# Kernel optimization log

Hardware: AMD Instinct MI355X
Metric: run time of the kernel (lower is better)

Reference implementation:

```python
import jax, jax.numpy as jnp
import numpy as np

EPS = 1e-12  # F.normalize default eps


def _l2norm(x):
    n = jnp.linalg.norm(x, axis=-1, keepdims=True)
    return x / jnp.maximum(n, EPS)


def setup_inputs() -> dict:
    key = jax.random.key(0)
    ks = jax.random.split(key, 6)
    B, N, d = 1024, 131072, 256
    query = jax.random.normal(ks[0], (B, d), dtype=jnp.float32)
    keys = jax.random.normal(ks[1], (N, d), dtype=jnp.float32)
    values = jax.random.normal(ks[2], (N, d), dtype=jnp.float32)
    quality_scores = jax.random.uniform(ks[3], (N,), dtype=jnp.float32)
    W = jax.random.normal(ks[4], (d, d), dtype=jnp.float32) / np.sqrt(d)
    b = jnp.zeros((d,), dtype=jnp.float32)
    temperature = jnp.asarray(0.02, dtype=jnp.float32)
    return {"query": query, "keys": keys, "values": values,
            "quality_scores": quality_scores, "W": W, "b": b,
            "temperature": temperature, "top_k": 32}


def reference(query, keys, values, quality_scores, W, b, temperature, top_k):
    # query_transform: nn.Linear -> x @ W.T + b
    q_t = query @ W.T + b                      # [B, d]
    qn = _l2norm(q_t)                          # [B, d]
    kn = _l2norm(keys)                         # [N, d]
    sim = (qn @ kn.T) / temperature            # [B, N]
    sim = sim + quality_scores[None, :] * 0.1  # quality boost
    top_vals, indices = jax.lax.top_k(sim, top_k)   # [B, k]
    scores = jax.nn.softmax(top_vals, axis=-1)      # [B, k]
    retrieved_keys = keys[indices]             # [B, k, d] gather
    retrieved_values = values[indices]         # [B, k, d]
    weighted_keys = jnp.einsum('bk,bkd->bd', scores, retrieved_keys)[:, None, :]
    weighted_values = jnp.einsum('bk,bkd->bd', scores, retrieved_values)[:, None, :]
    return weighted_keys, weighted_values, scores
```

## Files before the change

### kernel.cpp

```cpp
#include <hip/hip_runtime.h>
#include <cstdint>
#include <cstddef>

#define B_Q   1024
#define N_K   131072
#define DIM   256
#define TOPK  32
#define EPSN  1e-12f

#define NRANGES 16
#define QGROUPS 16
#define QT      64
#define WQ      8
#define NT      1024
#define NTILES  8
#define CAP     160
#define FLUSH_AT 96

typedef unsigned long long u64;
typedef unsigned int u32;

__global__ __launch_bounds__(256) void qn_kernel(
    const float* __restrict__ query, const float* __restrict__ W,
    const float* __restrict__ b, float* __restrict__ qn) {
  const int row = blockIdx.x;
  const int j   = threadIdx.x;
  __shared__ float4 qrow[64];
  __shared__ float red[256];
  if (j < 64) qrow[j] = ((const float4*)(query + (size_t)row * DIM))[j];
  __syncthreads();
  const float4* W4 = (const float4*)(W + (size_t)j * DIM);
  float acc = b[j];
  #pragma unroll 8
  for (int kk = 0; kk < 64; ++kk) {
    float4 w = W4[kk];
    float4 qv = qrow[kk];
    acc = fmaf(qv.x, w.x, acc);
    acc = fmaf(qv.y, w.y, acc);
    acc = fmaf(qv.z, w.z, acc);
    acc = fmaf(qv.w, w.w, acc);
  }
  red[j] = acc * acc;
  __syncthreads();
  #pragma unroll
  for (int s = 128; s > 0; s >>= 1) {
    if (j < s) red[j] += red[j + s];
    __syncthreads();
  }
  float norm = sqrtf(red[0]);
  qn[(size_t)row * DIM + j] = acc / fmaxf(norm, EPSN);
}

__global__ __launch_bounds__(256) void knorm_kernel(
    const float* __restrict__ keys, const float* __restrict__ quality,
    const float* __restrict__ temperature,
    float* __restrict__ scale, float* __restrict__ boost) {
  const int tid = threadIdx.x;
  const int lane = tid & 63;
  const int row = blockIdx.x * 4 + (tid >> 6);
  float4 v = ((const float4*)(keys + (size_t)row * DIM))[lane];
  float ss = v.x * v.x + v.y * v.y + v.z * v.z + v.w * v.w;
  #pragma unroll
  for (int off = 32; off > 0; off >>= 1) ss += __shfl_xor(ss, off, 64);
  if (lane == 0) {
    float norm = sqrtf(ss);
    scale[row] = 1.0f / (fmaxf(norm, EPSN) * temperature[0]);
    boost[row] = 0.1f * quality[row];
  }
}

__device__ __attribute__((noinline)) float wave_extract(
    float2* list, int n, int lane, float2* gout) {
  float v0 = -INFINITY, v1 = -INFINITY, v2 = -INFINITY;
  float i0 = 0.f, i1 = 0.f, i2 = 0.f;
  if (lane < n)        { float2 e = list[lane];       v0 = e.x; i0 = e.y; }
  if (lane + 64 < n)   { float2 e = list[lane + 64];  v1 = e.x; i1 = e.y; }
  if (lane + 128 < n)  { float2 e = list[lane + 128]; v2 = e.x; i2 = e.y; }
  float m = -INFINITY;
  #pragma unroll 1
  for (int it = 0; it < TOPK; ++it) {
    float lm = fmaxf(v0, fmaxf(v1, v2));
    m = lm;
    #pragma unroll
    for (int off = 32; off > 0; off >>= 1) m = fmaxf(m, __shfl_xor(m, off, 64));
    u64 msk = __ballot(lm == m);
    int first = __ffsll((unsigned long long)msk) - 1;
    if (lane == first) {
      float2 e;
      if (v0 == lm)      { e = make_float2(v0, i0); v0 = -INFINITY; }
      else if (v1 == lm) { e = make_float2(v1, i1); v1 = -INFINITY; }
      else               { e = make_float2(v2, i2); v2 = -INFINITY; }
      if (gout) gout[it] = e; else list[it] = e;
    }
  }
  return m;
}

__device__ __forceinline__ void gload_lds16(const float* __restrict__ g, void* l) {
  __builtin_amdgcn_global_load_lds(
      (const __attribute__((address_space(1))) void*)g,
      (__attribute__((address_space(3))) void*)l, 16, 0, 0);
}

__device__ __forceinline__ void stage_chunk(
    const float* __restrict__ keys, long nbase, int tile, int chunk,
    float4* kb, int tid) {
  const long nrow0 = nbase + (long)tile * NT + tid;
  const float* s0 = keys + (nrow0 << 8) + (chunk << 2);
  gload_lds16(s0, kb + tid);
  gload_lds16(s0 + (512L << 8), kb + tid + 512);
}

__global__ __launch_bounds__(512, 2) void sim_topk_kernel(
    const float* __restrict__ qn, const float* __restrict__ keys,
    const float* __restrict__ scale, const float* __restrict__ boost,
    float2* __restrict__ glists,
    float2* __restrict__ partials)
{
  const int tid  = threadIdx.x;
  const int lane = tid & 63;
  const int wid  = __builtin_amdgcn_readfirstlane(tid >> 6);
  const int rg = blockIdx.x;
  const int qg = blockIdx.y;
  const int qbase = qg * QT + wid * WQ;
  const long nbase = (long)rg * (N_K / NRANGES);

  __shared__ float4 kbuf[2][NT];
  __shared__ float  qbuf[QT * DIM];
  __shared__ int cnt[QT];

  if (tid < QT) cnt[tid] = 0;

  {
    const float* qsrc = qn + (size_t)(qg * QT) * DIM;
    #pragma unroll
    for (int it = 0; it < 8; ++it)
      gload_lds16(qsrc + (size_t)(it * 512 + tid) * 4, qbuf + (it * 512 + tid) * 4);
  }
  int buf = 0;
  stage_chunk(keys, nbase, 0, 0, &kbuf[0][0], tid);

  float tau_r[WQ];
  #pragma unroll
  for (int qi = 0; qi < WQ; ++qi) tau_r[qi] = -INFINITY;
  float2* const mybase = glists + ((size_t)qbase * NRANGES + rg) * CAP;

  #pragma unroll 1
  for (int t = 0; t < NTILES; ++t) {
    float acc[WQ][16];
    #pragma unroll
    for (int qi = 0; qi < WQ; ++qi)
      #pragma unroll
      for (int j = 0; j < 16; ++j) acc[qi][j] = 0.f;

    #pragma unroll 1
    for (int c = 0; c < 64; ++c) {
      __syncthreads();
      if (c < 63)                stage_chunk(keys, nbase, t,     c + 1, &kbuf[buf ^ 1][0], tid);
      else if (t < NTILES - 1)   stage_chunk(keys, nbase, t + 1, 0,     &kbuf[buf ^ 1][0], tid);
      float4 qv[WQ];
      #pragma unroll
      for (int qi = 0; qi < WQ; ++qi)
        qv[qi] = *(const float4*)&qbuf[(wid * WQ + qi) * DIM + c * 4];
      #pragma unroll
      for (int j = 0; j < 16; ++j) {
        float4 kv = kbuf[buf][j * 64 + lane];
        #pragma unroll
        for (int qi = 0; qi < WQ; ++qi) {
          acc[qi][j] = fmaf(qv[qi].x, kv.x, acc[qi][j]);
          acc[qi][j] = fmaf(qv[qi].y, kv.y, acc[qi][j]);
          acc[qi][j] = fmaf(qv[qi].z, kv.z, acc[qi][j]);
          acc[qi][j] = fmaf(qv[qi].w, kv.w, acc[qi][j]);
        }
      }
      buf ^= 1;
    }

    const int ntile0 = t * NT;
    #pragma unroll
    for (int j = 0; j < 16; ++j) {
      const int nloc = ntile0 + j * 64 + lane;
      const long ng = nbase + nloc;
      const float sc = scale[ng];
      const float bo = boost[ng];
      bool any = false;
      #pragma unroll
      for (int qi = 0; qi < WQ; ++qi) {
        float v = fmaf(acc[qi][j], sc, bo);
        bool p = v > tau_r[qi];
        any |= p;
        if (p) {
          int pos = atomicAdd(&cnt[wid * WQ + qi], 1);
          mybase[(size_t)qi * NRANGES * CAP + pos] = make_float2(v, __int_as_float((int)ng));
        }
      }
      if (__any(any)) {
        #pragma unroll
        for (int qi = 0; qi < WQ; ++qi) {
          int cc = cnt[wid * WQ + qi];
          if (cc > FLUSH_AT) {
            tau_r[qi] = wave_extract(mybase + (size_t)qi * NRANGES * CAP, cc, lane, nullptr);
            if (lane == 0) cnt[wid * WQ + qi] = TOPK;
          }
        }
      }
    }
  }

  #pragma unroll 1
  for (int qi = 0; qi < WQ; ++qi) {
    float2* out = partials + ((size_t)(qbase + qi) * NRANGES + rg) * TOPK;
    wave_extract(mybase + (size_t)qi * NRANGES * CAP, cnt[wid * WQ + qi], lane, out);
  }
}

__device__ __forceinline__ u32 f2ord(float f) {
  u32 u = __float_as_uint(f);
  return (u & 0x80000000u) ? ~u : (u | 0x80000000u);
}
__device__ __forceinline__ float ord2f(u32 o) {
  u32 u = (o & 0x80000000u) ? (o ^ 0x80000000u) : ~o;
  return __uint_as_float(u);
}

__global__ __launch_bounds__(256) void merge_kernel(
    const float2* __restrict__ partials, const float* __restrict__ keys,
    const float* __restrict__ values, float* __restrict__ out) {
  const int q = blockIdx.x;
  const int tid = threadIdx.x;
  __shared__ u64 skey[NRANGES * TOPK];
  for (int i = tid; i < 512; i += 256) {
    float2 e = partials[(size_t)q * 512 + i];
    int idx = __float_as_int(e.y);
    skey[i] = ((u64)f2ord(e.x) << 32) | (u32)(~(u32)idx);
  }
  __syncthreads();
  for (int k = 2; k <= 512; k <<= 1) {
    for (int jj = k >> 1; jj > 0; jj >>= 1) {
      for (int i = tid; i < 512; i += 256) {
        int ixj = i ^ jj;
        if (ixj > i) {
          u64 a = skey[i], bb = skey[ixj];
          bool up = ((i & k) == 0);
          if ((a < bb) == up) { skey[i] = bb; skey[ixj] = a; }
        }
      }
      __syncthreads();
    }
  }
  __shared__ float sval[TOPK];
  __shared__ int   sidx[TOPK];
  __shared__ float sscore[TOPK];
  if (tid < TOPK) {
    u64 kk = skey[tid];
    sval[tid] = ord2f((u32)(kk >> 32));
    sidx[tid] = (int)(~(u32)(kk & 0xffffffffu));
  }
  __syncthreads();
  if (tid < TOPK) {
    float m = sval[0];
    float e = expf(sval[tid] - m);
    float s = e;
    #pragma unroll
    for (int off = 16; off > 0; off >>= 1) s += __shfl_xor(s, off, 64);
    sscore[tid] = e / s;
  }
  __syncthreads();
  if (tid < TOPK) out[(size_t)2 * B_Q * DIM + (size_t)q * TOPK + tid] = sscore[tid];
  float wk = 0.f, wv = 0.f;
  #pragma unroll 4
  for (int kk2 = 0; kk2 < TOPK; ++kk2) {
    float s = sscore[kk2];
    size_t idr = (size_t)sidx[kk2] * DIM + tid;
    wk = fmaf(s, keys[idr], wk);
    wv = fmaf(s, values[idr], wv);
  }
  out[(size_t)q * DIM + tid] = wk;
  out[(size_t)B_Q * DIM + (size_t)q * DIM + tid] = wv;
}

extern "C" void kernel_launch(void* const* d_in, const int* in_sizes, int n_in,
                              void* d_out, int out_size, void* d_ws, size_t ws_size,
                              hipStream_t stream) {
  const float* query   = (const float*)d_in[0];
  const float* keys    = (const float*)d_in[1];
  const float* values  = (const float*)d_in[2];
  const float* quality = (const float*)d_in[3];
  const float* W       = (const float*)d_in[4];
  const float* b       = (const float*)d_in[5];
  const float* temp    = (const float*)d_in[6];
  float* out = (float*)d_out;
  float* ws = (float*)d_ws;

  float* qn    = ws;
  float* scale = ws + 262144;
  float* boost = ws + 393216;
  float2* partials = (float2*)(ws + 524288);
  float2* glists   = (float2*)(ws + 524288 + 1048576);

  hipLaunchKernelGGL(qn_kernel, dim3(B_Q), dim3(256), 0, stream, query, W, b, qn);
  hipLaunchKernelGGL(knorm_kernel, dim3(N_K / 4), dim3(256), 0, stream,
                     keys, quality, temp, scale, boost);
  hipLaunchKernelGGL(sim_topk_kernel, dim3(NRANGES, QGROUPS), dim3(512), 0, stream,
                     qn, keys, scale, boost, glists, partials);
  hipLaunchKernelGGL(merge_kernel, dim3(B_Q), dim3(256), 0, stream,
                     partials, keys, values, out);
}
```

Baseline: 2.060 ms.

## Shrink sim-topk tiles to 32 queries x 512 keys with 256-thread blocks

Reshapes the similarity/top-k kernel so each block handles 32 queries and 512-key tiles with 256 threads. Each pipeline phase now stages two 4-float chunks (8 dims), which halves the number of barriers per tile, and the accumulator array per thread shrinks from 16 to 8 keys per query. The grid doubles in the query dimension, giving more blocks and lower register pressure, but each key tile is now reloaded by twice as many query groups, doubling key traffic from global memory.

Result: faster. 1.994 ms (-3.2%).

```diff
diff --git a/kernel.cpp b/kernel.cpp
--- a/kernel.cpp
+++ b/kernel.cpp
@@ -9,11 +9,11 @@
 #define EPSN  1e-12f
 
 #define NRANGES 16
-#define QGROUPS 16
-#define QT      64
+#define QGROUPS 32
+#define QT      32
 #define WQ      8
-#define NT      1024
-#define NTILES  8
+#define NT      512
+#define NTILES  16
 #define CAP     160
 #define FLUSH_AT 96
 
@@ -102,16 +102,19 @@
       (__attribute__((address_space(3))) void*)l, 16, 0, 0);
 }
 
-__device__ __forceinline__ void stage_chunk(
-    const float* __restrict__ keys, long nbase, int tile, int chunk,
+__device__ __forceinline__ void stage_phase(
+    const float* __restrict__ keys, long nbase, int t, int c,
     float4* kb, int tid) {
-  const long nrow0 = nbase + (long)tile * NT + tid;
-  const float* s0 = keys + (nrow0 << 8) + (chunk << 2);
-  gload_lds16(s0, kb + tid);
-  gload_lds16(s0 + (512L << 8), kb + tid + 512);
-}
-
-__global__ __launch_bounds__(512, 2) void sim_topk_kernel(
+  #pragma unroll
+  for (int i = 0; i < 4; ++i) {
+    const int c2   = i >> 1;
+    const int keyl = (i & 1) * 256 + tid;
+    const float* src = keys + ((size_t)(nbase + t * NT + keyl) << 8) + c * 8 + c2 * 4;
+    gload_lds16(src, kb + c2 * 512 + keyl);
+  }
+}
+
+__global__ __launch_bounds__(256, 2) void sim_topk_kernel(
     const float* __restrict__ qn, const float* __restrict__ keys,
     const float* __restrict__ scale, const float* __restrict__ boost,
     float2* __restrict__ glists,
@@ -123,9 +126,10 @@
   const int rg = blockIdx.x;
   const int qg = blockIdx.y;
   const int qbase = qg * QT + wid * WQ;
+  const int qloc0 = wid * WQ;
   const long nbase = (long)rg * (N_K / NRANGES);
 
-  __shared__ float4 kbuf[2][NT];
+  __shared__ float4 kbuf4[2][2 * NT];
   __shared__ float  qbuf[QT * DIM];
   __shared__ int cnt[QT];
 
@@ -135,10 +139,10 @@
     const float* qsrc = qn + (size_t)(qg * QT) * DIM;
     #pragma unroll
     for (int it = 0; it < 8; ++it)
-      gload_lds16(qsrc + (size_t)(it * 512 + tid) * 4, qbuf + (it * 512 + tid) * 4);
+      gload_lds16(qsrc + (size_t)(it * 256 + tid) * 4, qbuf + (it * 256 + tid) * 4);
   }
   int buf = 0;
-  stage_chunk(keys, nbase, 0, 0, &kbuf[0][0], tid);
+  stage_phase(keys, nbase, 0, 0, &kbuf4[0][0], tid);
 
   float tau_r[WQ];
   #pragma unroll
@@ -147,30 +151,33 @@
 
   #pragma unroll 1
   for (int t = 0; t < NTILES; ++t) {
-    float acc[WQ][16];
+    float acc[WQ][8];
     #pragma unroll
     for (int qi = 0; qi < WQ; ++qi)
       #pragma unroll
-      for (int j = 0; j < 16; ++j) acc[qi][j] = 0.f;
+      for (int j = 0; j < 8; ++j) acc[qi][j] = 0.f;
 
     #pragma unroll 1
-    for (int c = 0; c < 64; ++c) {
+    for (int c = 0; c < 32; ++c) {
       __syncthreads();
-      if (c < 63)                stage_chunk(keys, nbase, t,     c + 1, &kbuf[buf ^ 1][0], tid);
-      else if (t < NTILES - 1)   stage_chunk(keys, nbase, t + 1, 0,     &kbuf[buf ^ 1][0], tid);
-      float4 qv[WQ];
+      if (c < 31)                stage_phase(keys, nbase, t,     c + 1, &kbuf4[buf ^ 1][0], tid);
+      else if (t < NTILES - 1)   stage_phase(keys, nbase, t + 1, 0,     &kbuf4[buf ^ 1][0], tid);
       #pragma unroll
-      for (int qi = 0; qi < WQ; ++qi)
-        qv[qi] = *(const float4*)&qbuf[(wid * WQ + qi) * DIM + c * 4];
-      #pragma unroll
-      for (int j = 0; j < 16; ++j) {
-        float4 kv = kbuf[buf][j * 64 + lane];
+      for (int c2 = 0; c2 < 2; ++c2) {
+        float4 qv[WQ];
         #pragma unroll
-        for (int qi = 0; qi < WQ; ++qi) {
-          acc[qi][j] = fmaf(qv[qi].x, kv.x, acc[qi][j]);
-          acc[qi][j] = fmaf(qv[qi].y, kv.y, acc[qi][j]);
-          acc[qi][j] = fmaf(qv[qi].z, kv.z, acc[qi][j]);
-          acc[qi][j] = fmaf(qv[qi].w, kv.w, acc[qi][j]);
+        for (int qi = 0; qi < WQ; ++qi)
+          qv[qi] = *(const float4*)&qbuf[(qloc0 + qi) * DIM + c * 8 + c2 * 4];
+        #pragma unroll
+        for (int j = 0; j < 8; ++j) {
+          float4 kv = kbuf4[buf][c2 * 512 + j * 64 + lane];
+          #pragma unroll
+          for (int qi = 0; qi < WQ; ++qi) {
+            acc[qi][j] = fmaf(qv[qi].x, kv.x, acc[qi][j]);
+            acc[qi][j] = fmaf(qv[qi].y, kv.y, acc[qi][j]);
+            acc[qi][j] = fmaf(qv[qi].z, kv.z, acc[qi][j]);
+            acc[qi][j] = fmaf(qv[qi].w, kv.w, acc[qi][j]);
+          }
         }
       }
       buf ^= 1;
@@ -178,7 +185,7 @@
 
     const int ntile0 = t * NT;
     #pragma unroll
-    for (int j = 0; j < 16; ++j) {
+    for (int j = 0; j < 8; ++j) {
       const int nloc = ntile0 + j * 64 + lane;
       const long ng = nbase + nloc;
       const float sc = scale[ng];
@@ -301,7 +308,7 @@
   hipLaunchKernelGGL(qn_kernel, dim3(B_Q), dim3(256), 0, stream, query, W, b, qn);
   hipLaunchKernelGGL(knorm_kernel, dim3(N_K / 4), dim3(256), 0, stream,
                      keys, quality, temp, scale, boost);
-  hipLaunchKernelGGL(sim_topk_kernel, dim3(NRANGES, QGROUPS), dim3(512), 0, stream,
+  hipLaunchKernelGGL(sim_topk_kernel, dim3(NRANGES, QGROUPS), dim3(256), 0, stream,
                      qn, keys, scale, boost, glists, partials);
   hipLaunchKernelGGL(merge_kernel, dim3(B_Q), dim3(256), 0, stream,
                      partials, keys, values, out);
```
